# Kernel tuning notes

Measured on AMD Instinct MI355X. Metric: run time of the kernel, lower is better.

## Reference

```python
import jax, jax.numpy as jnp
import numpy as np

K_NODES = 512  # per-expert capacity (k_nodes init arg)


def setup_inputs() -> dict:
    key = jax.random.key(0)
    k1, k2, k3, k4 = jax.random.split(key, 4)
    B_T, D, E = 16384, 512, 64
    x = jax.random.normal(k1, (B_T, D, 2), jnp.float32)
    # gate: orthogonal_(gain=0.1) ~ small-scale dense matrix
    gate_weights = jax.random.normal(k2, (2 * D, E), jnp.float32) * (0.1 / np.sqrt(2 * D))
    # ComplexKaimingInitializer: |N(0,1)|/sqrt(fan_in) magnitude, uniform phase
    mag = jnp.abs(jax.random.normal(k3, (E, D, D), jnp.float32)) / np.sqrt(D)
    phase = jax.random.uniform(k4, (E, D, D), jnp.float32, minval=0.0, maxval=2.0 * np.pi)
    experts_w = jnp.stack([mag * jnp.cos(phase), mag * jnp.sin(phase)], axis=-1)  # [E,D,D,2]
    act_bias = jnp.zeros((D,), jnp.float32)
    return {"x": x, "gate_weights": gate_weights, "experts_w": experts_w, "act_bias": act_bias}


def reference(x, gate_weights, experts_w, act_bias):
    # x: [B_T, D, 2] interleaved-real tokens
    B_T, D, _ = x.shape
    E = gate_weights.shape[1]
    k = min(B_T, K_NODES)

    # --- expert-choice routing: each expert picks its top-k tokens ---
    scores = jnp.nan_to_num(x.reshape(B_T, 2 * D) @ gate_weights)  # [B_T, E]
    topk_scores, topk_idx = jax.lax.top_k(scores.T, k)             # [E, k] each

    # --- gather tokens per expert (row-major [E, k] order, as in forward()) ---
    flat_gather = topk_idx.reshape(-1)                  # [E*k]
    xb = x[flat_gather].reshape(E, k, D, 2)             # [E, k, D, 2]
    xr, xi = xb[..., 0], xb[..., 1]
    wr, wi = experts_w[..., 0], experts_w[..., 1]

    # --- grouped complex GEMM as 4 real batched matmuls ---
    yr = jnp.einsum('ekd,edf->ekf', xr, wr) - jnp.einsum('ekd,edf->ekf', xi, wi)
    yi = jnp.einsum('ekd,edf->ekf', xr, wi) + jnp.einsum('ekd,edf->ekf', xi, wr)
    y = jnp.nan_to_num(jnp.stack([yr, yi], axis=-1))    # [E, k, D, 2]

    # weight by routing scores, then scatter-add combine
    y_weighted = (y * topk_scores[..., None, None]).reshape(E * k, D, 2)
    # NOTE: original code scatters with topk_indices.T.reshape(-1) (column-major
    # w.r.t. the [E,k] gather order). Reproduced faithfully.
    flat_scatter = topk_idx.T.reshape(-1)               # [E*k]
    out = jnp.zeros((B_T, D, 2), jnp.float32).at[flat_scatter].add(y_weighted)
    counts = jnp.zeros((B_T,), jnp.float32).at[flat_scatter].add(1.0)
    agg = out / jnp.maximum(counts, 1.0)[:, None, None]

    # ComplexGELU: exact (erf) GELU on real/imag parts with shared bias
    res = jax.nn.gelu(agg + act_bias[:, None], approximate=False)  # [B_T, D, 2]
    return res
```

## Files before the change

kernel.cpp:

```cpp
#include <hip/hip_runtime.h>
#include <stdint.h>
#include <math.h>

typedef uint32_t u32;
typedef uint64_t u64;
typedef unsigned short u16;

#define B_T    16384
#define DD     512
#define NE     64
#define KCAP   512
#define TWO_D  1024

typedef __attribute__((ext_vector_type(8))) short bf16x8;
typedef __attribute__((ext_vector_type(4))) float f32x4;
typedef __attribute__((ext_vector_type(4))) u32 u32x4;

static __device__ __forceinline__ u32 mono_of(float s) {
  u32 b = __float_as_uint(s);
  return (b & 0x80000000u) ? ~b : (b | 0x80000000u);
}
static __device__ __forceinline__ float score_from_mono(u32 m) {
  u32 b = (m & 0x80000000u) ? (m ^ 0x80000000u) : ~m;
  return __uint_as_float(b);
}
static __device__ __forceinline__ u16 f2bf(float f) {
  u32 b = __float_as_uint(f);
  b += 0x7FFFu + ((b >> 16) & 1u);
  return (u16)(b >> 16);
}
static __device__ __forceinline__ u32 f2bf2(float lo, float hi) {
  return (u32)f2bf(lo) | ((u32)f2bf(hi) << 16);
}
static __device__ __forceinline__ float bf2f(u32 u) {
  return __uint_as_float(u << 16);
}
static __device__ __forceinline__ u32 cvtpk(float lo, float hi) {
  u32 r;
  asm("v_cvt_pk_bf16_f32 %0, %1, %2" : "=v"(r) : "v"(lo), "v"(hi));
  return r;
}
static __device__ __forceinline__ void gload_lds16(const u16* g, u16* l) {
  __builtin_amdgcn_global_load_lds(
      (const __attribute__((address_space(1))) u32*)(g),
      (__attribute__((address_space(3))) u32*)(l), 16, 0, 0);
}
static __device__ __forceinline__ bf16x8 negbf8(bf16x8 v) {
  u32x4 u;
  u32x4 s = *reinterpret_cast<u32x4*>(&v);
  u[0] = s[0] ^ 0x80008000u;
  u[1] = s[1] ^ 0x80008000u;
  u[2] = s[2] ^ 0x80008000u;
  u[3] = s[3] ^ 0x80008000u;
  return *reinterpret_cast<bf16x8*>(&u);
}

__global__ __launch_bounds__(256) void k0_xconv(const float* __restrict__ x,
                                                u16* __restrict__ xrb,
                                                u16* __restrict__ xib) {
  int idx = blockIdx.x * 256 + threadIdx.x;
  float4 v = reinterpret_cast<const float4*>(x)[idx];
  reinterpret_cast<u32*>(xrb)[idx] = f2bf2(v.x, v.z);
  reinterpret_cast<u32*>(xib)[idx] = f2bf2(v.y, v.w);
}

__global__ __launch_bounds__(256) void k1_gate(const float* __restrict__ x,
                                               const float* __restrict__ gw,
                                               float* __restrict__ scoresT) {
  __shared__ __align__(16) float xs[128][32];
  __shared__ __align__(16) float gs[128][64];
  const int tb  = blockIdx.x * 32;
  const int tid = threadIdx.x;
  const int tx = tid & 7, ty = tid >> 3;

  float accC[2][4];
  float accT[2][4];
#pragma unroll
  for (int i = 0; i < 2; ++i)
#pragma unroll
    for (int j = 0; j < 4; ++j) { accC[i][j] = 0.f; accT[i][j] = 0.f; }

  for (int c = 0; c < 8; ++c) {
    const int k0 = c * 128;
    {
      const int t = tid & 31, ks = (tid >> 5) * 16;
      const float* src = x + (size_t)(tb + t) * TWO_D + k0 + ks;
#pragma unroll
      for (int i = 0; i < 4; ++i) {
        float4 v = reinterpret_cast<const float4*>(src)[i];
        xs[ks + i * 4 + 0][t] = v.x;
        xs[ks + i * 4 + 1][t] = v.y;
        xs[ks + i * 4 + 2][t] = v.z;
        xs[ks + i * 4 + 3][t] = v.w;
      }
      const float4* gsrc = reinterpret_cast<const float4*>(gw + (size_t)k0 * 64);
      float4* gdst = reinterpret_cast<float4*>(&gs[0][0]);
#pragma unroll
      for (int i = 0; i < 8; ++i) gdst[tid + i * 256] = gsrc[tid + i * 256];
    }
    __syncthreads();
    for (int k = 0; k < 128; ++k) {
      float4 a4 = *reinterpret_cast<float4*>(&xs[k][tx * 4]);
      float2 b2 = *reinterpret_cast<float2*>(&gs[k][ty * 2]);
      float av[4] = {a4.x, a4.y, a4.z, a4.w};
      float bv[2] = {b2.x, b2.y};
#pragma unroll
      for (int i = 0; i < 2; ++i)
#pragma unroll
        for (int j = 0; j < 4; ++j) accC[i][j] = fmaf(bv[i], av[j], accC[i][j]);
    }
    __syncthreads();
    if (c == 3 || c == 7) {
#pragma unroll
      for (int i = 0; i < 2; ++i)
#pragma unroll
        for (int j = 0; j < 4; ++j) {
          accT[i][j] = accT[i][j] + accC[i][j];
          accC[i][j] = 0.f;
        }
    }
  }
#pragma unroll
  for (int i = 0; i < 2; ++i) {
    float4 v = make_float4(accT[i][0], accT[i][1], accT[i][2], accT[i][3]);
    *reinterpret_cast<float4*>(&scoresT[(size_t)(ty * 2 + i) * B_T + tb + tx * 4]) = v;
  }
}

__global__ __launch_bounds__(1024) void k2_topk(const float* __restrict__ scoresT,
                                                int* __restrict__ topk_idx,
                                                float* __restrict__ topk_scr,
                                                int* __restrict__ counts,
                                                int* __restrict__ entries) {
  const int e = blockIdx.x, tid = threadIdx.x;
  const float* row = scoresT + (size_t)e * B_T;
  __shared__ u32 keys[B_T];
  __shared__ u32 hist[256];
  __shared__ u32 s_prefix, s_r;
  __shared__ u32 cnt_gt, cnt_eq;
  __shared__ u64 skey[512];
  __shared__ u32 tie[512];

#pragma unroll
  for (int i = 0; i < 4; ++i) {
    int v4 = i * 1024 + tid;
    float4 v = reinterpret_cast<const float4*>(row)[v4];
    keys[v4 * 4 + 0] = mono_of(v.x);
    keys[v4 * 4 + 1] = mono_of(v.y);
    keys[v4 * 4 + 2] = mono_of(v.z);
    keys[v4 * 4 + 3] = mono_of(v.w);
  }
  if (tid == 0) { s_prefix = 0; s_r = KCAP; cnt_gt = 0; cnt_eq = 0; }
  u32 prefmask = 0;
  __syncthreads();

  for (int pass = 0; pass < 4; ++pass) {
    const int shift = 24 - 8 * pass;
    if (tid < 256) hist[tid] = 0;
    __syncthreads();
    const u32 prefix = s_prefix;
    for (int t = tid; t < B_T; t += 1024) {
      u32 m = keys[t];
      if ((m & prefmask) == prefix) atomicAdd(&hist[(m >> shift) & 0xFFu], 1u);
    }
    __syncthreads();
    if (tid == 0) {
      u32 r = s_r, cum = 0;
      int sel = 0;
      for (int b = 255; b >= 0; --b) {
        if (cum + hist[b] >= r) { sel = b; s_r = r - cum; break; }
        cum += hist[b];
      }
      s_prefix = prefix | ((u32)sel << shift);
    }
    prefmask |= (0xFFu << shift);
    __syncthreads();
  }

  const u32 kmono = s_prefix;
  const u32 rneed = s_r;

  for (int t = tid; t < B_T; t += 1024) {
    u32 m = keys[t];
    if (m > kmono) {
      u32 p = atomicAdd(&cnt_gt, 1u);
      if (p < 512) skey[p] = ((u64)(~m) << 32) | (u32)t;
    } else if (m == kmono) {
      u32 p = atomicAdd(&cnt_eq, 1u);
      if (p < 512) tie[p] = (u32)t;
    }
  }
  __syncthreads();

  const u32 ngt = cnt_gt;
  const u32 ne = cnt_eq < 512u ? cnt_eq : 512u;
  if (tid < ne) {
    u32 my = tie[tid];
    u32 rank = 0;
    for (u32 j = 0; j < ne; ++j) rank += (tie[j] < my) ? 1u : 0u;
    if (rank < rneed) skey[ngt + rank] = ((u64)(~kmono) << 32) | my;
  }
  __syncthreads();

  if (tid < 512) {
    u64 my = skey[tid];
    u32 rank = 0;
    for (int j = 0; j < 512; ++j) rank += (skey[j] < my) ? 1u : 0u;
    u32 idx = (u32)my;
    u32 m = ~((u32)(my >> 32));
    topk_idx[e * KCAP + rank] = (int)idx;
    topk_scr[e * KCAP + rank] = score_from_mono(m);
    int pos = atomicAdd(&counts[idx], 1);
    entries[idx * 64 + pos] = (int)(rank * 64 + e);
  }
}

__global__ __launch_bounds__(256) void k3_wtrans(const float* __restrict__ w,
                                                 u16* __restrict__ wrT,
                                                 u16* __restrict__ wiT) {
  __shared__ float2 tr[32][33];
  const int bid = blockIdx.x;
  const int e = bid >> 8, tile = bid & 255;
  const int d0 = (tile >> 4) * 32, f0 = (tile & 15) * 32;
  const int tid = threadIdx.x;
  const int fl2 = tid & 15, dl0 = tid >> 4;
  const float* base = w + ((size_t)e * 512 + d0) * 1024 + (size_t)f0 * 2;
#pragma unroll
  for (int it = 0; it < 2; ++it) {
    int dl = dl0 + it * 16;
    float4 v = *reinterpret_cast<const float4*>(base + (size_t)dl * 1024 + fl2 * 4);
    tr[dl][fl2 * 2]     = make_float2(v.x, v.y);
    tr[dl][fl2 * 2 + 1] = make_float2(v.z, v.w);
  }
  __syncthreads();
  const int d2 = (tid & 15) * 2, fl0 = tid >> 4;
#pragma unroll
  for (int it = 0; it < 2; ++it) {
    int f = fl0 + it * 16;
    float2 a = tr[d2][f], b = tr[d2 + 1][f];
    size_t off = ((size_t)e * 512 + f0 + f) * 512 + d0 + d2;
    *reinterpret_cast<u32*>(&wrT[off]) = f2bf2(a.x, b.x);
    *reinterpret_cast<u32*>(&wiT[off]) = f2bf2(a.y, b.y);
  }
}

__global__ __launch_bounds__(256, 2) void k4_pre(
    const u16* __restrict__ xrb, const u16* __restrict__ xib,
    const int* __restrict__ topk_idx, const float* __restrict__ topk_scr,
    const u16* __restrict__ wrT, const u16* __restrict__ wiT,
    u16* __restrict__ yrw, u16* __restrict__ yiw) {
  const int bid = blockIdx.x;
  const int xcd = bid & 7, q = bid >> 3, t = q & 15, g = q >> 4;
  const int e = g * 8 + xcd;
  const int mb = t & 3, fb = t >> 2;
  const int m0 = mb * 128, f0 = fb * 128;

  __shared__ __align__(16) u16 Ar[2][4096];
  __shared__ __align__(16) u16 Ai[2][4096];
  __shared__ __align__(16) u16 Bu[2][4096];
  __shared__ __align__(16) u16 Bv[2][4096];
  __shared__ int tok[128];
  __shared__ float scr[128];

  const int tid = threadIdx.x;
  if (tid < 128) {
    tok[tid] = topk_idx[e * KCAP + m0 + tid];
    scr[tid] = topk_scr[e * KCAP + m0 + tid];
  }
  __syncthreads();

  const int r0  = tid & 127;
  const int ka0 = (tid >> 7) * 8;
  const int ka1 = ka0 + 16;
  const size_t brow = ((size_t)e * 512 + f0 + r0) * 512;
  const size_t arow = (size_t)tok[r0] * 512;
  const int wv = tid >> 6, ln = tid & 63;
  const int d0 = wv * 512;
  const int d1 = 2048 + wv * 512;

  const int mbase = (wv >> 1) * 64, nbase = (wv & 1) * 64;
  const int frow = ln & 15, fq = ln >> 4;
  const int ra = fq * 1024 + (mbase + frow) * 8;
  const int rb = fq * 1024 + (nbase + frow) * 8;

  f32x4 accR[4][4] = {};
  f32x4 accI[4][4] = {};

#define STAGE(b, kk)                                         \
  do {                                                       \
    gload_lds16(wrT + brow + (kk) + ka0, Bu[b] + d0);        \
    gload_lds16(wrT + brow + (kk) + ka1, Bu[b] + d1);        \
    gload_lds16(wiT + brow + (kk) + ka0, Bv[b] + d0);        \
    gload_lds16(wiT + brow + (kk) + ka1, Bv[b] + d1);        \
    gload_lds16(xrb + arow + (kk) + ka0, Ar[b] + d0);        \
    gload_lds16(xrb + arow + (kk) + ka1, Ar[b] + d1);        \
    gload_lds16(xib + arow + (kk) + ka0, Ai[b] + d0);        \
    gload_lds16(xib + arow + (kk) + ka1, Ai[b] + d1);        \
  } while (0)

  STAGE(0, 0);
  __syncthreads();

  for (int s = 0; s < 16; ++s) {
    const int b = s & 1;
    if (s < 15) STAGE(b ^ 1, (s + 1) * 32);

    bf16x8 ar[4], ai[4], bu[4], bv[4];
#pragma unroll
    for (int m = 0; m < 4; ++m) {
      ar[m] = *reinterpret_cast<const bf16x8*>(&Ar[b][ra + m * 128]);
      ai[m] = *reinterpret_cast<const bf16x8*>(&Ai[b][ra + m * 128]);
    }
#pragma unroll
    for (int n = 0; n < 4; ++n) {
      bu[n] = *reinterpret_cast<const bf16x8*>(&Bu[b][rb + n * 128]);
      bv[n] = *reinterpret_cast<const bf16x8*>(&Bv[b][rb + n * 128]);
    }
#pragma unroll
    for (int m = 0; m < 4; ++m)
#pragma unroll
      for (int n = 0; n < 4; ++n) {
        bf16x8 bw = negbf8(bv[n]);
        accR[m][n] = __builtin_amdgcn_mfma_f32_16x16x32_bf16(ar[m], bu[n], accR[m][n], 0, 0, 0);
        accR[m][n] = __builtin_amdgcn_mfma_f32_16x16x32_bf16(ai[m], bw,    accR[m][n], 0, 0, 0);
        accI[m][n] = __builtin_amdgcn_mfma_f32_16x16x32_bf16(ar[m], bv[n], accI[m][n], 0, 0, 0);
        accI[m][n] = __builtin_amdgcn_mfma_f32_16x16x32_bf16(ai[m], bu[n], accI[m][n], 0, 0, 0);
      }
    __syncthreads();
  }
#undef STAGE

  const int rr = fq * 4;
#pragma unroll
  for (int m = 0; m < 4; ++m) {
#pragma unroll
    for (int r = 0; r < 4; ++r) {
      const int jl = mbase + m * 16 + rr + r;
      const float ww = scr[jl];
      const size_t ybase = ((size_t)e * KCAP + m0 + jl) * DD;
#pragma unroll
      for (int n = 0; n < 4; ++n) {
        const int fg = f0 + nbase + n * 16 + frow;
        yrw[ybase + fg] = f2bf(accR[m][n][r] * ww);
        yiw[ybase + fg] = f2bf(accI[m][n][r] * ww);
      }
    }
  }
}

__global__ __launch_bounds__(256, 2) void k4_fb(
    const float* __restrict__ x, const int* __restrict__ topk_idx,
    const float* __restrict__ topk_scr, const u16* __restrict__ wrT,
    const u16* __restrict__ wiT, u16* __restrict__ yrw, u16* __restrict__ yiw) {
  const int bid = blockIdx.x;
  const int xcd = bid & 7, q = bid >> 3, t = q & 15, g = q >> 4;
  const int e = g * 8 + xcd;
  const int mb = t & 3, fb = t >> 2;
  const int m0 = mb * 128, f0 = fb * 128;

  __shared__ __align__(16) u16 Ar[4096];
  __shared__ __align__(16) u16 Ai[4096];
  __shared__ __align__(16) u16 Bu[4096];
  __shared__ __align__(16) u16 Bv[4096];
  __shared__ int tok[128];
  __shared__ float scr[128];

  const int tid = threadIdx.x;
  if (tid < 128) {
    tok[tid] = topk_idx[e * KCAP + m0 + tid];
    scr[tid] = topk_scr[e * KCAP + m0 + tid];
  }
  __syncthreads();

  const int r0  = tid & 127;
  const int ka0 = (tid >> 7) * 8;
  const int ka1 = ka0 + 16;
  const size_t brow = ((size_t)e * 512 + f0 + r0) * 512;
  const int wv = tid >> 6, ln = tid & 63;
  const int d0 = wv * 512;
  const int d1 = 2048 + wv * 512;

  const int row = tid >> 1, half = tid & 1;
  const float* arow_f = x + (size_t)tok[row] * TWO_D + half * 32;

  const int mbase = (wv >> 1) * 64, nbase = (wv & 1) * 64;
  const int frow = ln & 15, fq = ln >> 4;
  const int ra = fq * 1024 + (mbase + frow) * 8;
  const int rb = fq * 1024 + (nbase + frow) * 8;

  f32x4 accR[4][4] = {};
  f32x4 accI[4][4] = {};

  for (int step = 0; step < 16; ++step) {
    const int k0 = step * 32;
    gload_lds16(wrT + brow + k0 + ka0, Bu + d0);
    gload_lds16(wrT + brow + k0 + ka1, Bu + d1);
    gload_lds16(wiT + brow + k0 + ka0, Bv + d0);
    gload_lds16(wiT + brow + k0 + ka1, Bv + d1);
    {
      const float4* ap = reinterpret_cast<const float4*>(arow_f + (size_t)k0 * 2);
      u32 xr[8], xi[8];
#pragma unroll
      for (int i = 0; i < 8; ++i) {
        float4 v = ap[i];
        xr[i] = cvtpk(v.x, v.z);
        xi[i] = cvtpk(v.y, v.w);
      }
      uint4 wa, wb;
      wa.x = xr[0]; wa.y = xr[1]; wa.z = xr[2]; wa.w = xr[3];
      wb.x = xr[4]; wb.y = xr[5]; wb.z = xr[6]; wb.w = xr[7];
      *reinterpret_cast<uint4*>(&Ar[(2 * half) * 1024 + row * 8]) = wa;
      *reinterpret_cast<uint4*>(&Ar[(2 * half + 1) * 1024 + row * 8]) = wb;
      wa.x = xi[0]; wa.y = xi[1]; wa.z = xi[2]; wa.w = xi[3];
      wb.x = xi[4]; wb.y = xi[5]; wb.z = xi[6]; wb.w = xi[7];
      *reinterpret_cast<uint4*>(&Ai[(2 * half) * 1024 + row * 8]) = wa;
      *reinterpret_cast<uint4*>(&Ai[(2 * half + 1) * 1024 + row * 8]) = wb;
    }
    __syncthreads();

    bf16x8 ar[4], ai[4], bu[4], bv[4];
#pragma unroll
    for (int m = 0; m < 4; ++m) {
      ar[m] = *reinterpret_cast<const bf16x8*>(&Ar[ra + m * 128]);
      ai[m] = *reinterpret_cast<const bf16x8*>(&Ai[ra + m * 128]);
    }
#pragma unroll
    for (int n = 0; n < 4; ++n) {
      bu[n] = *reinterpret_cast<const bf16x8*>(&Bu[rb + n * 128]);
      bv[n] = *reinterpret_cast<const bf16x8*>(&Bv[rb + n * 128]);
    }
#pragma unroll
    for (int m = 0; m < 4; ++m)
#pragma unroll
      for (int n = 0; n < 4; ++n) {
        bf16x8 bw = negbf8(bv[n]);
        accR[m][n] = __builtin_amdgcn_mfma_f32_16x16x32_bf16(ar[m], bu[n], accR[m][n], 0, 0, 0);
        accR[m][n] = __builtin_amdgcn_mfma_f32_16x16x32_bf16(ai[m], bw,    accR[m][n], 0, 0, 0);
        accI[m][n] = __builtin_amdgcn_mfma_f32_16x16x32_bf16(ar[m], bv[n], accI[m][n], 0, 0, 0);
        accI[m][n] = __builtin_amdgcn_mfma_f32_16x16x32_bf16(ai[m], bu[n], accI[m][n], 0, 0, 0);
      }
    __syncthreads();
  }

  const int rr = fq * 4;
#pragma unroll
  for (int m = 0; m < 4; ++m) {
#pragma unroll
    for (int r = 0; r < 4; ++r) {
      const int jl = mbase + m * 16 + rr + r;
      const float ww = scr[jl];
      const size_t ybase = ((size_t)e * KCAP + m0 + jl) * DD;
#pragma unroll
      for (int n = 0; n < 4; ++n) {
        const int fg = f0 + nbase + n * 16 + frow;
        yrw[ybase + fg] = f2bf(accR[m][n][r] * ww);
        yiw[ybase + fg] = f2bf(accI[m][n][r] * ww);
      }
    }
  }
}

#define GELU(z) (0.5f * (z) * (1.0f + erff((z)*0.70710678118654752440f)))
__global__ __launch_bounds__(256) void k5_gather(
    const u16* __restrict__ yrw, const u16* __restrict__ yiw,
    const int* __restrict__ counts, const int* __restrict__ entries,
    const float* __restrict__ bias, float* __restrict__ out) {
  const int t = blockIdx.x;
  const int tid = threadIdx.x;
  const int c = counts[t];
  const float inv = 1.0f / (float)(c > 0 ? c : 1);
  const int f0 = tid * 2;
  float sr0 = 0.f, sr1 = 0.f, si0 = 0.f, si1 = 0.f;
  for (int i = 0; i < c; ++i) {
    int srcrow = entries[t * 64 + i];
    size_t off = (size_t)srcrow * DD + f0;
    u32 pr = *reinterpret_cast<const u32*>(yrw + off);
    u32 pi = *reinterpret_cast<const u32*>(yiw + off);
    sr0 += bf2f(pr & 0xFFFFu); sr1 += bf2f(pr >> 16);
    si0 += bf2f(pi & 0xFFFFu); si1 += bf2f(pi >> 16);
  }
  const float b0 = bias[f0], b1 = bias[f0 + 1];
  float v0 = sr0 * inv + b0;
  float v1 = si0 * inv + b0;
  float v2 = sr1 * inv + b1;
  float v3 = si1 * inv + b1;
  float4 o = make_float4(GELU(v0), GELU(v1), GELU(v2), GELU(v3));
  *reinterpret_cast<float4*>(&out[(size_t)t * TWO_D + f0 * 2]) = o;
}

extern "C" void kernel_launch(void* const* d_in, const int* in_sizes, int n_in,
                              void* d_out, int out_size, void* d_ws, size_t ws_size,
                              hipStream_t stream) {
  const float* x    = (const float*)d_in[0];
  const float* gw   = (const float*)d_in[1];
  const float* w    = (const float*)d_in[2];
  const float* bias = (const float*)d_in[3];
  float* out = (float*)d_out;

  char* ws = (char*)d_ws;
  u16*   yrw     = (u16*)(ws);
  float* scoresT = (float*)(ws);
  u16*   yiw     = (u16*)(ws + 33554432);
  int*   tidx    = (int*)(ws + 67108864);
  float* tscr    = (float*)(ws + 67239936);
  int*   counts  = (int*)(ws + 67371008);
  int*   entries = (int*)(ws + 67436544);
  u16*   wrT     = (u16*)(ws + 71630848);
  u16*   wiT     = (u16*)(ws + 105185280);
  u16*   xrb     = (u16*)(ws + 138739712);
  u16*   xib     = (u16*)(ws + 155516928);

  const bool preconv = ws_size >= 172294144ull;

  hipMemsetAsync(counts, 0, B_T * sizeof(int), stream);
  k1_gate<<<B_T / 32, 256, 0, stream>>>(x, gw, scoresT);
  k2_topk<<<NE, 1024, 0, stream>>>(scoresT, tidx, tscr, counts, entries);
  k3_wtrans<<<NE * 256, 256, 0, stream>>>(w, wrT, wiT);
  if (preconv) {
    k0_xconv<<<16384, 256, 0, stream>>>(x, xrb, xib);
    k4_pre<<<1024, 256, 0, stream>>>(xrb, xib, tidx, tscr, wrT, wiT, yrw, yiw);
  } else {
    k4_fb<<<1024, 256, 0, stream>>>(x, tidx, tscr, wrT, wiT, yrw, yiw);
  }
  k5_gather<<<B_T, 256, 0, stream>>>(yrw, yiw, counts, entries, bias, out);
}
```

Measured before the change: 290.7 us.

## Fuse x bf16 conversion into gate, widen transpose and gather, single-buffer GEMM

```diff
diff --git a/kernel.cpp b/kernel.cpp
--- a/kernel.cpp
+++ b/kernel.cpp
@@ -55,18 +55,11 @@
   return *reinterpret_cast<bf16x8*>(&u);
 }
 
-__global__ __launch_bounds__(256) void k0_xconv(const float* __restrict__ x,
-                                                u16* __restrict__ xrb,
-                                                u16* __restrict__ xib) {
-  int idx = blockIdx.x * 256 + threadIdx.x;
-  float4 v = reinterpret_cast<const float4*>(x)[idx];
-  reinterpret_cast<u32*>(xrb)[idx] = f2bf2(v.x, v.z);
-  reinterpret_cast<u32*>(xib)[idx] = f2bf2(v.y, v.w);
-}
-
 __global__ __launch_bounds__(256) void k1_gate(const float* __restrict__ x,
                                                const float* __restrict__ gw,
-                                               float* __restrict__ scoresT) {
+                                               float* __restrict__ scoresT,
+                                               u16* __restrict__ xrb,
+                                               u16* __restrict__ xib) {
   __shared__ __align__(16) float xs[128][32];
   __shared__ __align__(16) float gs[128][64];
   const int tb  = blockIdx.x * 32;
@@ -85,6 +78,7 @@
     {
       const int t = tid & 31, ks = (tid >> 5) * 16;
       const float* src = x + (size_t)(tb + t) * TWO_D + k0 + ks;
+      u32 rr[4], ii[4];
 #pragma unroll
       for (int i = 0; i < 4; ++i) {
         float4 v = reinterpret_cast<const float4*>(src)[i];
@@ -92,7 +86,16 @@
         xs[ks + i * 4 + 1][t] = v.y;
         xs[ks + i * 4 + 2][t] = v.z;
         xs[ks + i * 4 + 3][t] = v.w;
-      }
+        rr[i] = f2bf2(v.x, v.z);
+        ii[i] = f2bf2(v.y, v.w);
+      }
+      const size_t xoff = (size_t)(tb + t) * 512 + c * 64 + (ks >> 1);
+      uint4 wr, wi;
+      wr.x = rr[0]; wr.y = rr[1]; wr.z = rr[2]; wr.w = rr[3];
+      wi.x = ii[0]; wi.y = ii[1]; wi.z = ii[2]; wi.w = ii[3];
+      *reinterpret_cast<uint4*>(xrb + xoff) = wr;
+      *reinterpret_cast<uint4*>(xib + xoff) = wi;
+
       const float4* gsrc = reinterpret_cast<const float4*>(gw + (size_t)k0 * 64);
       float4* gdst = reinterpret_cast<float4*>(&gs[0][0]);
 #pragma unroll
@@ -218,29 +221,40 @@
 __global__ __launch_bounds__(256) void k3_wtrans(const float* __restrict__ w,
                                                  u16* __restrict__ wrT,
                                                  u16* __restrict__ wiT) {
-  __shared__ float2 tr[32][33];
+  __shared__ float fr[64][33];
+  __shared__ float fi[64][33];
   const int bid = blockIdx.x;
-  const int e = bid >> 8, tile = bid & 255;
-  const int d0 = (tile >> 4) * 32, f0 = (tile & 15) * 32;
+  const int e = bid >> 7, tile = bid & 127;
+  const int d0 = (tile >> 4) * 64, f0 = (tile & 15) * 32;
   const int tid = threadIdx.x;
-  const int fl2 = tid & 15, dl0 = tid >> 4;
-  const float* base = w + ((size_t)e * 512 + d0) * 1024 + (size_t)f0 * 2;
-#pragma unroll
-  for (int it = 0; it < 2; ++it) {
-    int dl = dl0 + it * 16;
-    float4 v = *reinterpret_cast<const float4*>(base + (size_t)dl * 1024 + fl2 * 4);
-    tr[dl][fl2 * 2]     = make_float2(v.x, v.y);
-    tr[dl][fl2 * 2 + 1] = make_float2(v.z, v.w);
+  {
+    const int row = tid >> 2, lane4 = tid & 3;
+    const float* src = w + ((size_t)(e * 512 + d0 + row)) * 1024 + f0 * 2 + lane4 * 16;
+#pragma unroll
+    for (int i = 0; i < 4; ++i) {
+      float4 v = reinterpret_cast<const float4*>(src)[i];
+      int fl = lane4 * 8 + 2 * i;
+      fr[row][fl] = v.x;      fi[row][fl] = v.y;
+      fr[row][fl + 1] = v.z;  fi[row][fl + 1] = v.w;
+    }
   }
   __syncthreads();
-  const int d2 = (tid & 15) * 2, fl0 = tid >> 4;
-#pragma unroll
-  for (int it = 0; it < 2; ++it) {
-    int f = fl0 + it * 16;
-    float2 a = tr[d2][f], b = tr[d2 + 1][f];
-    size_t off = ((size_t)e * 512 + f0 + f) * 512 + d0 + d2;
-    *reinterpret_cast<u32*>(&wrT[off]) = f2bf2(a.x, b.x);
-    *reinterpret_cast<u32*>(&wiT[off]) = f2bf2(a.y, b.y);
+  {
+    const int f = tid >> 3, dg = tid & 7;
+    u32 pr[4], pi[4];
+#pragma unroll
+    for (int j = 0; j < 4; ++j) {
+      float r0 = fr[dg * 8 + 2 * j][f],     i0 = fi[dg * 8 + 2 * j][f];
+      float r1 = fr[dg * 8 + 2 * j + 1][f], i1 = fi[dg * 8 + 2 * j + 1][f];
+      pr[j] = f2bf2(r0, r1);
+      pi[j] = f2bf2(i0, i1);
+    }
+    const size_t off = ((size_t)e * 512 + f0 + f) * 512 + d0 + dg * 8;
+    uint4 vr, vi;
+    vr.x = pr[0]; vr.y = pr[1]; vr.z = pr[2]; vr.w = pr[3];
+    vi.x = pi[0]; vi.y = pi[1]; vi.z = pi[2]; vi.w = pi[3];
+    *reinterpret_cast<uint4*>(wrT + off) = vr;
+    *reinterpret_cast<uint4*>(wiT + off) = vi;
   }
 }
 
@@ -255,10 +269,10 @@
   const int mb = t & 3, fb = t >> 2;
   const int m0 = mb * 128, f0 = fb * 128;
 
-  __shared__ __align__(16) u16 Ar[2][4096];
-  __shared__ __align__(16) u16 Ai[2][4096];
-  __shared__ __align__(16) u16 Bu[2][4096];
-  __shared__ __align__(16) u16 Bv[2][4096];
+  __shared__ __align__(16) u16 Ar[4096];
+  __shared__ __align__(16) u16 Ai[4096];
+  __shared__ __align__(16) u16 Bu[4096];
+  __shared__ __align__(16) u16 Bv[4096];
   __shared__ int tok[128];
   __shared__ float scr[128];
 
@@ -286,35 +300,28 @@
   f32x4 accR[4][4] = {};
   f32x4 accI[4][4] = {};
 
-#define STAGE(b, kk)                                         \
-  do {                                                       \
-    gload_lds16(wrT + brow + (kk) + ka0, Bu[b] + d0);        \
-    gload_lds16(wrT + brow + (kk) + ka1, Bu[b] + d1);        \
-    gload_lds16(wiT + brow + (kk) + ka0, Bv[b] + d0);        \
-    gload_lds16(wiT + brow + (kk) + ka1, Bv[b] + d1);        \
-    gload_lds16(xrb + arow + (kk) + ka0, Ar[b] + d0);        \
-    gload_lds16(xrb + arow + (kk) + ka1, Ar[b] + d1);        \
-    gload_lds16(xib + arow + (kk) + ka0, Ai[b] + d0);        \
-    gload_lds16(xib + arow + (kk) + ka1, Ai[b] + d1);        \
-  } while (0)
-
-  STAGE(0, 0);
-  __syncthreads();
-
-  for (int s = 0; s < 16; ++s) {
-    const int b = s & 1;
-    if (s < 15) STAGE(b ^ 1, (s + 1) * 32);
+  for (int step = 0; step < 16; ++step) {
+    const int k0 = step * 32;
+    gload_lds16(wrT + brow + k0 + ka0, Bu + d0);
+    gload_lds16(wrT + brow + k0 + ka1, Bu + d1);
+    gload_lds16(wiT + brow + k0 + ka0, Bv + d0);
+    gload_lds16(wiT + brow + k0 + ka1, Bv + d1);
+    gload_lds16(xrb + arow + k0 + ka0, Ar + d0);
+    gload_lds16(xrb + arow + k0 + ka1, Ar + d1);
+    gload_lds16(xib + arow + k0 + ka0, Ai + d0);
+    gload_lds16(xib + arow + k0 + ka1, Ai + d1);
+    __syncthreads();
 
     bf16x8 ar[4], ai[4], bu[4], bv[4];
 #pragma unroll
     for (int m = 0; m < 4; ++m) {
-      ar[m] = *reinterpret_cast<const bf16x8*>(&Ar[b][ra + m * 128]);
-      ai[m] = *reinterpret_cast<const bf16x8*>(&Ai[b][ra + m * 128]);
+      ar[m] = *reinterpret_cast<const bf16x8*>(&Ar[ra + m * 128]);
+      ai[m] = *reinterpret_cast<const bf16x8*>(&Ai[ra + m * 128]);
     }
 #pragma unroll
     for (int n = 0; n < 4; ++n) {
-      bu[n] = *reinterpret_cast<const bf16x8*>(&Bu[b][rb + n * 128]);
-      bv[n] = *reinterpret_cast<const bf16x8*>(&Bv[b][rb + n * 128]);
+      bu[n] = *reinterpret_cast<const bf16x8*>(&Bu[rb + n * 128]);
+      bv[n] = *reinterpret_cast<const bf16x8*>(&Bv[rb + n * 128]);
     }
 #pragma unroll
     for (int m = 0; m < 4; ++m)
@@ -328,7 +335,6 @@
       }
     __syncthreads();
   }
-#undef STAGE
 
   const int rr = fq * 4;
 #pragma unroll
@@ -465,27 +471,31 @@
     const u16* __restrict__ yrw, const u16* __restrict__ yiw,
     const int* __restrict__ counts, const int* __restrict__ entries,
     const float* __restrict__ bias, float* __restrict__ out) {
-  const int t = blockIdx.x;
-  const int tid = threadIdx.x;
+  const int t = blockIdx.x * 2 + (threadIdx.x >> 7);
+  const int lane = threadIdx.x & 127;
   const int c = counts[t];
   const float inv = 1.0f / (float)(c > 0 ? c : 1);
-  const int f0 = tid * 2;
-  float sr0 = 0.f, sr1 = 0.f, si0 = 0.f, si1 = 0.f;
+  const int f4 = lane * 4;
+  float sr[4] = {0.f, 0.f, 0.f, 0.f}, si[4] = {0.f, 0.f, 0.f, 0.f};
   for (int i = 0; i < c; ++i) {
     int srcrow = entries[t * 64 + i];
-    size_t off = (size_t)srcrow * DD + f0;
-    u32 pr = *reinterpret_cast<const u32*>(yrw + off);
-    u32 pi = *reinterpret_cast<const u32*>(yiw + off);
-    sr0 += bf2f(pr & 0xFFFFu); sr1 += bf2f(pr >> 16);
-    si0 += bf2f(pi & 0xFFFFu); si1 += bf2f(pi >> 16);
-  }
-  const float b0 = bias[f0], b1 = bias[f0 + 1];
-  float v0 = sr0 * inv + b0;
-  float v1 = si0 * inv + b0;
-  float v2 = sr1 * inv + b1;
-  float v3 = si1 * inv + b1;
-  float4 o = make_float4(GELU(v0), GELU(v1), GELU(v2), GELU(v3));
-  *reinterpret_cast<float4*>(&out[(size_t)t * TWO_D + f0 * 2]) = o;
+    size_t off = (size_t)srcrow * DD + f4;
+    uint2 pr = *reinterpret_cast<const uint2*>(yrw + off);
+    uint2 pi = *reinterpret_cast<const uint2*>(yiw + off);
+    sr[0] += bf2f(pr.x & 0xFFFFu); sr[1] += bf2f(pr.x >> 16);
+    sr[2] += bf2f(pr.y & 0xFFFFu); sr[3] += bf2f(pr.y >> 16);
+    si[0] += bf2f(pi.x & 0xFFFFu); si[1] += bf2f(pi.x >> 16);
+    si[2] += bf2f(pi.y & 0xFFFFu); si[3] += bf2f(pi.y >> 16);
+  }
+  const float b0 = bias[f4], b1 = bias[f4 + 1], b2 = bias[f4 + 2], b3 = bias[f4 + 3];
+  float4 o1, o2;
+  o1.x = GELU(sr[0] * inv + b0); o1.y = GELU(si[0] * inv + b0);
+  o1.z = GELU(sr[1] * inv + b1); o1.w = GELU(si[1] * inv + b1);
+  o2.x = GELU(sr[2] * inv + b2); o2.y = GELU(si[2] * inv + b2);
+  o2.z = GELU(sr[3] * inv + b3); o2.w = GELU(si[3] * inv + b3);
+  float* dst = out + (size_t)t * TWO_D + (size_t)f4 * 2;
+  reinterpret_cast<float4*>(dst)[0] = o1;
+  reinterpret_cast<float4*>(dst)[1] = o2;
 }
 
 extern "C" void kernel_launch(void* const* d_in, const int* in_sizes, int n_in,
@@ -513,14 +523,17 @@
   const bool preconv = ws_size >= 172294144ull;
 
   hipMemsetAsync(counts, 0, B_T * sizeof(int), stream);
-  k1_gate<<<B_T / 32, 256, 0, stream>>>(x, gw, scoresT);
-  k2_topk<<<NE, 1024, 0, stream>>>(scoresT, tidx, tscr, counts, entries);
-  k3_wtrans<<<NE * 256, 256, 0, stream>>>(w, wrT, wiT);
   if (preconv) {
-    k0_xconv<<<16384, 256, 0, stream>>>(x, xrb, xib);
+    k1_gate<<<B_T / 32, 256, 0, stream>>>(x, gw, scoresT, xrb, xib);
+    k2_topk<<<NE, 1024, 0, stream>>>(scoresT, tidx, tscr, counts, entries);
+    k3_wtrans<<<NE * 128, 256, 0, stream>>>(w, wrT, wiT);
     k4_pre<<<1024, 256, 0, stream>>>(xrb, xib, tidx, tscr, wrT, wiT, yrw, yiw);
   } else {
+    k1_gate<<<B_T / 32, 256, 0, stream>>>(x, gw, scoresT, (u16*)(ws + 33554432),
+                                          (u16*)(ws + 33554432 + 16777216));
+    k2_topk<<<NE, 1024, 0, stream>>>(scoresT, tidx, tscr, counts, entries);
+    k3_wtrans<<<NE * 128, 256, 0, stream>>>(w, wrT, wiT);
     k4_fb<<<1024, 256, 0, stream>>>(x, tidx, tscr, wrT, wiT, yrw, yiw);
   }
-  k5_gather<<<B_T, 256, 0, stream>>>(yrw, yiw, counts, entries, bias, out);
-}
+  k5_gather<<<B_T / 2, 256, 0, stream>>>(yrw, yiw, counts, entries, bias, out);
+}
```

New measurement: 276.8 us (median of 2 runs). 1.05x faster.
